# Kernel optimization log

Hardware: AMD Instinct MI355X
Metric: run time of the kernel (lower is better)

The kernel has to match this reference:

```python
import jax, jax.numpy as jnp
import numpy as np

V, E, H = 32000, 256, 256  # vocab, embed dim, encoder hidden (decoder hidden = 2H)
B, S, T = 64, 32, 32


def gru_cell(x, h, W_ih, W_hh, b_ih, b_hh):
    # PyTorch GRU cell math. x: (B, in), h: (B, Hd)
    gi = x @ W_ih.T + b_ih
    gh = h @ W_hh.T + b_hh
    i_r, i_z, i_n = jnp.split(gi, 3, axis=-1)
    h_r, h_z, h_n = jnp.split(gh, 3, axis=-1)
    r = jax.nn.sigmoid(i_r + h_r)
    z = jax.nn.sigmoid(i_z + h_z)
    n = jnp.tanh(i_n + r * h_n)
    return (1.0 - z) * n + z * h


def setup_inputs() -> dict:
    key = jax.random.key(0)
    ks = jax.random.split(key, 20)
    s = 0.05
    emb_enc = jax.random.normal(ks[0], (V, E), jnp.float32) * s
    emb_enc = emb_enc.at[0].set(0.0)  # padding_idx=0
    emb_dec = jax.random.normal(ks[1], (V, E), jnp.float32) * s
    emb_dec = emb_dec.at[0].set(0.0)
    inp = {
        "src": jax.random.randint(ks[2], (B, S), 0, V),
        "trg": jax.random.randint(ks[3], (B, T), 0, V),
        "emb_enc": emb_enc,
        # encoder bidirectional GRU (single layer)
        "W_ih_f": jax.random.normal(ks[4], (3 * H, E), jnp.float32) * s,
        "W_hh_f": jax.random.normal(ks[5], (3 * H, H), jnp.float32) * s,
        "b_ih_f": jnp.zeros((3 * H,), jnp.float32),
        "b_hh_f": jnp.zeros((3 * H,), jnp.float32),
        "W_ih_b": jax.random.normal(ks[6], (3 * H, E), jnp.float32) * s,
        "W_hh_b": jax.random.normal(ks[7], (3 * H, H), jnp.float32) * s,
        "b_ih_b": jnp.zeros((3 * H,), jnp.float32),
        "b_hh_b": jnp.zeros((3 * H,), jnp.float32),
        "emb_dec": emb_dec,
        # decoder GRU: input E + 2H, hidden 2H
        "W_ih_d": jax.random.normal(ks[8], (3 * 2 * H, E + 2 * H), jnp.float32) * s,
        "W_hh_d": jax.random.normal(ks[9], (3 * 2 * H, 2 * H), jnp.float32) * s,
        "b_ih_d": jnp.zeros((3 * 2 * H,), jnp.float32),
        "b_hh_d": jnp.zeros((3 * 2 * H,), jnp.float32),
        "fc_W": jax.random.normal(ks[10], (V, 2 * H), jnp.float32) * s,
        "fc_b": jnp.zeros((V,), jnp.float32),
    }
    return inp


def _forward(src, trg, emb_enc, W_ih_f, W_hh_f, b_ih_f, b_hh_f,
             W_ih_b, W_hh_b, b_ih_b, b_hh_b, emb_dec,
             W_ih_d, W_hh_d, b_ih_d, b_hh_d, fc_W, fc_b):
    b, s = src.shape
    t = trg.shape[1]
    x = emb_enc[src]                      # (B,S,E)
    xs = jnp.swapaxes(x, 0, 1)            # (S,B,E)
    h0 = jnp.zeros((b, H), x.dtype)

    def fstep(h, xt):
        h = gru_cell(xt, h, W_ih_f, W_hh_f, b_ih_f, b_hh_f)
        return h, None

    def bstep(h, xt):
        h = gru_cell(xt, h, W_ih_b, W_hh_b, b_ih_b, b_hh_b)
        return h, None

    hf, _ = jax.lax.scan(fstep, h0, xs)
    hb, _ = jax.lax.scan(bstep, h0, xs[::-1])
    context = jnp.concatenate([hf, hb], axis=-1)   # (B,2H) = final bidir hidden

    # teacher_forcing_ratio = 1.0 -> decoder input at step t is trg[:, t-1]
    dec_in = jnp.swapaxes(trg[:, :-1], 0, 1)       # (T-1, B)

    def dstep(h, tok):
        xt = jnp.concatenate([emb_dec[tok], context], axis=-1)  # (B, E+2H)
        h = gru_cell(xt, h, W_ih_d, W_hh_d, b_ih_d, b_hh_d)
        logits = h @ fc_W.T + fc_b                              # (B, V)
        return h, logits

    _, logits = jax.lax.scan(dstep, context, dec_in)  # (T-1, B, V)
    logits = jnp.swapaxes(logits, 0, 1)                # (B, T-1, V)
    outputs = jnp.concatenate(
        [jnp.zeros((b, 1, fc_W.shape[0]), logits.dtype), logits], axis=1)
    return outputs


def reference(src, trg, emb_enc, W_ih_f, W_hh_f, b_ih_f, b_hh_f,
              W_ih_b, W_hh_b, b_ih_b, b_hh_b, emb_dec,
              W_ih_d, W_hh_d, b_ih_d, b_hh_d, fc_W, fc_b):
    return _forward(src, trg, emb_enc, W_ih_f, W_hh_f, b_ih_f, b_hh_f,
                    W_ih_b, W_hh_b, b_ih_b, b_hh_b, emb_dec,
                    W_ih_d, W_hh_d, b_ih_d, b_hh_d, fc_W, fc_b)
```

## Files before the change

### kernel.cpp

```cpp
#include <hip/hip_runtime.h>
#include <cmath>

typedef _Float16 f16;
typedef _Float16 f16x4 __attribute__((ext_vector_type(4)));
typedef _Float16 f16x8 __attribute__((ext_vector_type(8)));
typedef float f32x4 __attribute__((ext_vector_type(4)));
typedef unsigned u32x4 __attribute__((ext_vector_type(4)));
typedef unsigned long long u64;

static constexpr u64 SENT = 0xFFFFFFFFFFFFFFFFULL;

union V4 { u32x4 u; f16x8 h; };

static constexpr size_t OFF_WIHF = 0;
static constexpr size_t OFF_WHHF = OFF_WIHF + 768UL*256*2;
static constexpr size_t OFF_WIHB = OFF_WHHF + 768UL*256*2;
static constexpr size_t OFF_WHHB = OFF_WIHB + 768UL*256*2;
static constexpr size_t OFF_WIHD = OFF_WHHB + 768UL*256*2;
static constexpr size_t OFF_WHHD = OFF_WIHD + 1536UL*768*2;
static constexpr size_t OFF_FCW  = OFF_WHHD + 1536UL*512*2;
static constexpr size_t OFF_XENC = OFF_FCW  + 32000UL*512*2;
static constexpr size_t OFF_XDEC = OFF_XENC + 2048UL*256*2;
static constexpr size_t OFF_GIF  = OFF_XDEC + 1984UL*256*2;
static constexpr size_t OFF_GIB  = OFF_GIF  + 2048UL*768*4;
static constexpr size_t OFF_GITOK= OFF_GIB  + 2048UL*768*4;
static constexpr size_t OFF_CTX32= OFF_GITOK+ 1984UL*1536*4;
static constexpr size_t OFF_CTX16= OFF_CTX32+ 64UL*512*4;
static constexpr size_t OFF_HPP  = OFF_CTX16+ 64UL*512*2;
static constexpr size_t OFF_HALL = OFF_HPP  + 2UL*32*64*256*2;

__device__ __forceinline__ float sigmoidf_(float x) {
  return __builtin_amdgcn_rcpf(1.f + __expf(-x));
}
__device__ __forceinline__ float tanhf_(float x) {
  float xc = fminf(fmaxf(x, -10.f), 10.f);
  float e = __expf(2.f * xc);
  return (e - 1.f) * __builtin_amdgcn_rcpf(e + 1.f);
}

__device__ __forceinline__ void wait_vm0() {
  asm volatile("s_waitcnt vmcnt(0)" ::: "memory");
  __builtin_amdgcn_sched_barrier(0);
}
__device__ __forceinline__ void sth4(f16* p, float a, float b, float c, float d) {
  union { u64 u; f16 h[4]; } t;
  t.h[0] = (f16)a; t.h[1] = (f16)b; t.h[2] = (f16)c; t.h[3] = (f16)d;
  __hip_atomic_store((u64*)p, t.u, __ATOMIC_RELAXED, __HIP_MEMORY_SCOPE_AGENT);
}

__global__ void k_init(const int* __restrict__ srct, const int* __restrict__ trgt,
                       const float* __restrict__ embe, const float* __restrict__ embd,
                       const float* __restrict__ wihf, const float* __restrict__ whhf,
                       const float* __restrict__ wihb, const float* __restrict__ whhb,
                       const float* __restrict__ wihd, const float* __restrict__ whhd,
                       const float* __restrict__ fcw,
                       f16* dWihf, f16* dWhhf, f16* dWihb, f16* dWhhb,
                       f16* dWihd, f16* dWhhd, f16* dFcw,
                       f16* __restrict__ Xenc, f16* __restrict__ Xdec,
                       f16* __restrict__ hpp, f16* __restrict__ Hall,
                       float* __restrict__ out) {
  int b = blockIdx.x, tid = threadIdx.x;
  if (b < 1024) {
    long t = (long)b * 256 + tid;
    const long stride = 1024L * 256;
    for (long i = t; i < 4032L * 64; i += stride) {
      int row = (int)(i >> 6), j4 = (int)(i & 63);
      const float* e; f16* d; int tok;
      if (row < 2048) {
        int s = row >> 6, bb = row & 63;
        tok = srct[bb * 32 + s]; e = embe; d = Xenc + (long)row * 256;
      } else {
        int rd = row - 2048; int tt = rd >> 6, bb = rd & 63;
        tok = trgt[bb * 32 + tt]; e = embd; d = Xdec + (long)rd * 256;
      }
      float4 v = ((const float4*)(e + (long)tok * 256))[j4];
      f16x4 o; o.x = (f16)v.x; o.y = (f16)v.y; o.z = (f16)v.z; o.w = (f16)v.w;
      ((f16x4*)d)[j4] = o;
    }
    for (long i = t; i < 64L * 8000; i += stride) {
      long bb = i / 8000, j = i % 8000;
      ((float4*)(out + bb * 1024000L))[j] = make_float4(0.f, 0.f, 0.f, 0.f);
    }
    u64* H8 = (u64*)Hall;
    if (t < 253952) H8[t] = SENT;
    u64* P8 = (u64*)hpp;
    if (t < 4096) { P8[t] = 0ULL; P8[131072 + t] = 0ULL; }
    if (t < 126976) { P8[4096 + t] = SENT; P8[131072 + 4096 + t] = SENT; }
  } else {
    long cb = b - 1024;
    const long stride = 4672L * 256;
    for (long i = cb * 256 + tid; i < 4784128L; i += stride) {
      const float* s; f16* d; long j = i;
      if (j < 49152L)        { s = wihf; d = dWihf; }
      else if (j < 98304L)   { s = whhf; d = dWhhf; j -= 49152L; }
      else if (j < 147456L)  { s = wihb; d = dWihb; j -= 98304L; }
      else if (j < 196608L)  { s = whhb; d = dWhhb; j -= 147456L; }
      else if (j < 491520L)  { s = wihd; d = dWihd; j -= 196608L; }
      else if (j < 688128L)  { s = whhd; d = dWhhd; j -= 491520L; }
      else                   { s = fcw;  d = dFcw;  j -= 688128L; }
      float4 v = ((const float4*)s)[j];
      f16x4 o; o.x = (f16)v.x; o.y = (f16)v.y; o.z = (f16)v.z; o.w = (f16)v.w;
      ((f16x4*)d)[j] = o;
    }
  }
}

__device__ __forceinline__ void gemm_body(int bx, int by,
                                          const f16* __restrict__ A, int lda,
                                          const f16* __restrict__ B, int ldb,
                                          const float* __restrict__ bias,
                                          float* __restrict__ C, int ldc, int Ksteps) {
  int m0 = bx * 64, n0 = by * 64;
  int lane = threadIdx.x & 63, w = threadIdx.x >> 6;
  int ar = m0 + w * 16 + (lane & 15);
  int koff = (lane >> 4) * 8;
  f32x4 acc[4] = {};
  for (int ks = 0; ks < Ksteps; ks++) {
    f16x8 a = *(const f16x8*)(A + (size_t)ar * lda + ks * 32 + koff);
#pragma unroll
    for (int ni = 0; ni < 4; ni++) {
      const f16* bp = B + (size_t)(n0 + ni * 16 + (lane & 15)) * ldb + ks * 32 + koff;
      f16x8 bfr = *(const f16x8*)bp;
      acc[ni] = __builtin_amdgcn_mfma_f32_16x16x32_f16(a, bfr, acc[ni], 0, 0, 0);
    }
  }
  int dm = m0 + w * 16 + ((lane >> 4) << 2);
  int dn0 = n0 + (lane & 15);
#pragma unroll
  for (int ni = 0; ni < 4; ni++) {
    int n = dn0 + ni * 16;
    float bv = bias ? bias[n] : 0.f;
#pragma unroll
    for (int r = 0; r < 4; r++) C[(size_t)(dm + r) * ldc + n] = acc[ni][r] + bv;
  }
}

__global__ __launch_bounds__(256) void k_gi(const f16* __restrict__ Xenc, const f16* __restrict__ Xdec,
                                            const f16* __restrict__ Wf, const f16* __restrict__ Wb,
                                            const f16* __restrict__ Wd,
                                            const float* __restrict__ bf, const float* __restrict__ bb,
                                            float* __restrict__ giF, float* __restrict__ giB,
                                            float* __restrict__ giTok) {
  int b = blockIdx.x;
  if (b < 384)      gemm_body(b & 31, b >> 5, Xenc, 256, Wf, 256, bf, giF, 768, 8);
  else if (b < 768) { b -= 384; gemm_body(b & 31, b >> 5, Xenc, 256, Wb, 256, bb, giB, 768, 8); }
  else              { b -= 768; gemm_body(b % 31, b / 31, Xdec, 256, Wd, 768, nullptr, giTok, 1536, 8); }
}

__global__ __launch_bounds__(256, 1) void k_enc(
    const float* __restrict__ giF, const float* __restrict__ giB,
    const f16* __restrict__ WhhF, const f16* __restrict__ WhhB,
    const float* __restrict__ bhhF, const float* __restrict__ bhhB,
    f16* __restrict__ hpp, float* __restrict__ ctx32, f16* __restrict__ ctx16) {
  __shared__ f16 W[96 * 256];
  int wg = blockIdx.x;
  int dir = wg >> 3, ns = wg & 7;
  int tid = threadIdx.x, lane = tid & 63, wv = tid >> 6;
  int mTile = wv;
  const float* gi = dir ? giB : giF;
  const f16* Whh = dir ? WhhB : WhhF;
  const float* bhh = dir ? bhhB : bhhF;
  f16* hb = hpp + (size_t)dir * (32 * 64 * 256);
  int lo = lane & 15, hi = lane >> 4;
  int m = mTile * 16 + lo;
  int jb0 = ns * 32 + hi * 4;

#pragma unroll
  for (int c = 0; c < 12; c++) {
    int seg = c * 256 + tid;
    int row = seg >> 5, ck = seg & 31;
    int q = row >> 5, ii = row & 31;
    f16x8 v = *(const f16x8*)(Whh + (size_t)(q * 256 + ns * 32 + ii) * 256 + ck * 8);
    int col = (ck * 8) ^ ((row & 7) << 3);
    *(f16x8*)&W[row * 256 + col] = v;
  }
  __syncthreads();

  float4 bh[3][2];
#pragma unroll
  for (int q = 0; q < 3; q++)
#pragma unroll
    for (int i = 0; i < 2; i++)
      bh[q][i] = *(const float4*)(bhh + q * 256 + jb0 + i * 16);

  float4 ho[2] = {};
  float4 gcur[3][2];
  {
    int s0 = dir ? 31 : 0;
    const float* g0 = gi + (size_t)s0 * (64 * 768);
#pragma unroll
    for (int q = 0; q < 3; q++)
#pragma unroll
      for (int i = 0; i < 2; i++)
        gcur[q][i] = *(const float4*)(g0 + (size_t)m * 768 + q * 256 + jb0 + i * 16);
  }

  for (int s = 0; s < 32; s++) {
    V4 hv[8];
    const char* hb8 = (const char*)hb + ((size_t)s * 16384 + (size_t)m * 256 + hi * 8) * 2;
    for (;;) {
#pragma unroll
      for (int ks = 0; ks < 8; ks++)
        asm volatile("global_load_dwordx4 %0, %1, off offset:%2 sc0 sc1"
                     : "=&v"(hv[ks].u) : "v"(hb8), "i"(ks * 64));
      wait_vm0();
      unsigned bad = 0;
#pragma unroll
      for (int ks = 0; ks < 8; ks++) {
        bad |= ((hv[ks].u.x & hv[ks].u.y) == 0xFFFFFFFFu);
        bad |= ((hv[ks].u.z & hv[ks].u.w) == 0xFFFFFFFFu);
      }
      if (!__any((int)bad)) break;
      __builtin_amdgcn_s_sleep(1);
    }
    f32x4 acc[3][2] = {};
#pragma unroll
    for (int ks = 0; ks < 8; ks++) {
#pragma unroll
      for (int q = 0; q < 3; q++)
#pragma unroll
        for (int i = 0; i < 2; i++) {
          int row = q * 32 + i * 16 + lo;
          int col = (ks * 32 + hi * 8) ^ ((row & 7) << 3);
          f16x8 w = *(const f16x8*)&W[row * 256 + col];
          acc[q][i] = __builtin_amdgcn_mfma_f32_16x16x32_f16(w, hv[ks].h, acc[q][i], 0, 0, 0);
        }
    }
#pragma unroll
    for (int i = 0; i < 2; i++) {
      float hvv[4];
#pragma unroll
      for (int r2 = 0; r2 < 4; r2++) {
        float rg = sigmoidf_(((const float*)&gcur[0][i])[r2] + acc[0][i][r2] + ((const float*)&bh[0][i])[r2]);
        float zg = sigmoidf_(((const float*)&gcur[1][i])[r2] + acc[1][i][r2] + ((const float*)&bh[1][i])[r2]);
        float ng = tanhf_(((const float*)&gcur[2][i])[r2] + rg * (acc[2][i][r2] + ((const float*)&bh[2][i])[r2]));
        float hprev = ((const float*)&ho[i])[r2];
        hvv[r2] = (1.f - zg) * ng + zg * hprev;
        ((float*)&ho[i])[r2] = hvv[r2];
      }
      if (s < 31) sth4(hb + (size_t)(s + 1) * 16384 + m * 256 + jb0 + i * 16,
                       hvv[0], hvv[1], hvv[2], hvv[3]);
    }
    if (s < 31) {
      int sn = s + 1;
      int sgin = dir ? (31 - sn) : sn;
      const float* gs = gi + (size_t)sgin * (64 * 768);
#pragma unroll
      for (int q = 0; q < 3; q++)
#pragma unroll
        for (int i = 0; i < 2; i++)
          gcur[q][i] = *(const float4*)(gs + (size_t)m * 768 + q * 256 + jb0 + i * 16);
    }
  }
#pragma unroll
  for (int i = 0; i < 2; i++) {
    int c = dir * 256 + jb0 + i * 16;
    *(float4*)(ctx32 + m * 512 + c) = ho[i];
    union { u64 u; f16 h[4]; } t;
#pragma unroll
    for (int r2 = 0; r2 < 4; r2++) t.h[r2] = (f16)((const float*)&ho[i])[r2];
    *(u64*)(ctx16 + m * 512 + c) = t.u;
  }
}

__global__ __launch_bounds__(256, 1) void k_dec(
    const float* __restrict__ giTok, const f16* __restrict__ Wihd, const float* __restrict__ bihd,
    const f16* __restrict__ Whh, const float* __restrict__ bhh,
    const float* __restrict__ ctx32, const f16* __restrict__ ctx16,
    f16* __restrict__ Hall) {
  __shared__ f16 W[48 * 512];
  int cg = blockIdx.x;
  int tid = threadIdx.x, lane = tid & 63, wv = tid >> 6;
  int mTile = wv;
  int lo = lane & 15, hi = lane >> 4;
  int koff = hi * 8;
  int m = mTile * 16 + lo;
  int j0 = cg * 16 + hi * 4;

#pragma unroll
  for (int c = 0; c < 12; c++) {
    int seg = c * 256 + tid;
    int row = seg >> 6, ck = seg & 63;
    int q = row >> 4, ii = row & 15;
    f16x8 v = *(const f16x8*)(Whh + (size_t)(q * 512 + cg * 16 + ii) * 512 + ck * 8);
    int col = (ck * 8) ^ ((row & 7) << 3);
    *(f16x8*)&W[row * 512 + col] = v;
  }

  f32x4 acx[3] = {};
#pragma unroll
  for (int ks = 0; ks < 16; ks++) {
    f16x8 a = *(const f16x8*)(ctx16 + (size_t)m * 512 + ks * 32 + koff);
#pragma unroll
    for (int q = 0; q < 3; q++) {
      f16x8 w = *(const f16x8*)(Wihd + (size_t)(q * 512 + cg * 16 + lo) * 768 + 256 + ks * 32 + koff);
      acx[q] = __builtin_amdgcn_mfma_f32_16x16x32_f16(w, a, acx[q], 0, 0, 0);
    }
  }
  float b0[4], b1[4], bo2[4], bhn[4];
#pragma unroll
  for (int r2 = 0; r2 < 4; r2++) {
    b0[r2]  = acx[0][r2] + bihd[j0 + r2]        + bhh[j0 + r2];
    b1[r2]  = acx[1][r2] + bihd[512 + j0 + r2]  + bhh[512 + j0 + r2];
    bo2[r2] = acx[2][r2] + bihd[1024 + j0 + r2];
    bhn[r2] = bhh[1024 + j0 + r2];
  }
  float4 ho = *(const float4*)(ctx32 + m * 512 + j0);
  float4 gcur[3];
#pragma unroll
  for (int q = 0; q < 3; q++)
    gcur[q] = *(const float4*)(giTok + (size_t)m * 1536 + q * 512 + j0);
  __syncthreads();

  for (int t = 0; t < 31; t++) {
    V4 hv[16];
    if (t == 0) {
      const char* cb = (const char*)ctx16 + ((size_t)m * 512 + hi * 8) * 2;
#pragma unroll
      for (int ks = 0; ks < 16; ks++)
        hv[ks].u = *(const u32x4*)(cb + ks * 64);
    } else {
      const char* hb8 = (const char*)Hall + ((size_t)(t - 1) * 32768 + (size_t)m * 512 + hi * 8) * 2;
      for (;;) {
#pragma unroll
        for (int ks = 0; ks < 16; ks++)
          asm volatile("global_load_dwordx4 %0, %1, off offset:%2 sc0 sc1"
                       : "=&v"(hv[ks].u) : "v"(hb8), "i"(ks * 64));
        wait_vm0();
        unsigned bad = 0;
#pragma unroll
        for (int ks = 0; ks < 16; ks++) {
          bad |= ((hv[ks].u.x & hv[ks].u.y) == 0xFFFFFFFFu);
          bad |= ((hv[ks].u.z & hv[ks].u.w) == 0xFFFFFFFFu);
        }
        if (!__any((int)bad)) break;
        __builtin_amdgcn_s_sleep(1);
      }
    }
    f32x4 acc[3] = {};
#pragma unroll
    for (int ks = 0; ks < 16; ks++) {
#pragma unroll
      for (int q = 0; q < 3; q++) {
        int row = q * 16 + lo;
        int col = (ks * 32 + hi * 8) ^ ((row & 7) << 3);
        f16x8 w = *(const f16x8*)&W[row * 512 + col];
        acc[q] = __builtin_amdgcn_mfma_f32_16x16x32_f16(w, hv[ks].h, acc[q], 0, 0, 0);
      }
    }
    float hvv[4];
#pragma unroll
    for (int r2 = 0; r2 < 4; r2++) {
      float rg = sigmoidf_(((const float*)&gcur[0])[r2] + acc[0][r2] + b0[r2]);
      float zg = sigmoidf_(((const float*)&gcur[1])[r2] + acc[1][r2] + b1[r2]);
      float ng = tanhf_(((const float*)&gcur[2])[r2] + bo2[r2] + rg * (acc[2][r2] + bhn[r2]));
      float hprev = ((const float*)&ho)[r2];
      hvv[r2] = (1.f - zg) * ng + zg * hprev;
      ((float*)&ho)[r2] = hvv[r2];
    }
    sth4(Hall + (size_t)t * 32768 + (size_t)m * 512 + j0, hvv[0], hvv[1], hvv[2], hvv[3]);
    {
      int tn = (t + 1 < 31) ? t + 1 : 30;
      const float* gs = giTok + (size_t)tn * (64 * 1536);
#pragma unroll
      for (int q = 0; q < 3; q++)
        gcur[q] = *(const float4*)(gs + (size_t)m * 1536 + q * 512 + j0);
    }
  }
}

__global__ __launch_bounds__(256, 2) void k_fc(const f16* __restrict__ Hall, const f16* __restrict__ Wfc,
                                               const float* __restrict__ fcb, float* __restrict__ out) {
  __shared__ f16 As[128 * 64];
  __shared__ f16 Bs[128 * 64];
  int bid = blockIdx.x;
  int bx = bid >> 4;
  int by = bid & 15;
  int m0 = by * 128, n0 = bx * 128;
  int tid = threadIdx.x, lane = tid & 63, wv = tid >> 6;
  int wm = wv >> 1, wn = wv & 1;
  f32x4 acc[4][4] = {};
  for (int kk = 0; kk < 8; kk++) {
    f16x8 ra[4], rb[4];
#pragma unroll
    for (int c = 0; c < 4; c++) {
      int seg = c * 256 + tid;
      int row = seg >> 3, ko = (seg & 7) * 8;
      ra[c] = *(const f16x8*)(Hall + (size_t)(m0 + row) * 512 + kk * 64 + ko);
      rb[c] = *(const f16x8*)(Wfc + (size_t)(n0 + row) * 512 + kk * 64 + ko);
    }
    __syncthreads();
#pragma unroll
    for (int c = 0; c < 4; c++) {
      int seg = c * 256 + tid;
      int row = seg >> 3;
      int col = ((seg & 7) * 8) ^ ((row & 7) << 3);
      *(f16x8*)&As[row * 64 + col] = ra[c];
      *(f16x8*)&Bs[row * 64 + col] = rb[c];
    }
    __syncthreads();
#pragma unroll
    for (int ks = 0; ks < 2; ks++) {
      f16x8 af[4], bf[4];
#pragma unroll
      for (int mi = 0; mi < 4; mi++) {
        int row = wm * 64 + mi * 16 + (lane & 15);
        int col = (ks * 32 + (lane >> 4) * 8) ^ ((row & 7) << 3);
        af[mi] = *(const f16x8*)&As[row * 64 + col];
      }
#pragma unroll
      for (int ni = 0; ni < 4; ni++) {
        int row = wn * 64 + ni * 16 + (lane & 15);
        int col = (ks * 32 + (lane >> 4) * 8) ^ ((row & 7) << 3);
        bf[ni] = *(const f16x8*)&Bs[row * 64 + col];
      }
#pragma unroll
      for (int mi = 0; mi < 4; mi++) {
#pragma unroll
        for (int ni = 0; ni < 4; ni++)
          acc[mi][ni] = __builtin_amdgcn_mfma_f32_16x16x32_f16(af[mi], bf[ni], acc[mi][ni], 0, 0, 0);
      }
    }
  }
  int dn0 = n0 + wn * 64 + (lane & 15);
  float bv[4];
#pragma unroll
  for (int ni = 0; ni < 4; ni++) bv[ni] = fcb[dn0 + ni * 16];
#pragma unroll
  for (int mi = 0; mi < 4; mi++) {
    int mbase = m0 + wm * 64 + mi * 16 + ((lane >> 4) << 2);
#pragma unroll
    for (int rr = 0; rr < 4; rr++) {
      int mm = mbase + rr;
      if (mm < 1984) {
        int t = mm >> 6, bb = mm & 63;
        float* orow = out + (size_t)bb * 1024000 + (size_t)(t + 1) * 32000;
#pragma unroll
        for (int ni = 0; ni < 4; ni++)
          __builtin_nontemporal_store(acc[mi][ni][rr] + bv[ni], orow + dn0 + ni * 16);
      }
    }
  }
}

extern "C" void kernel_launch(void* const* d_in, const int* in_sizes, int n_in,
                              void* d_out, int out_size, void* d_ws, size_t ws_size,
                              hipStream_t stream) {
  const int*   srct = (const int*)d_in[0];
  const int*   trgt = (const int*)d_in[1];
  const float* embe = (const float*)d_in[2];
  const float* wihf = (const float*)d_in[3];
  const float* whhf = (const float*)d_in[4];
  const float* bihf = (const float*)d_in[5];
  const float* bhhf = (const float*)d_in[6];
  const float* wihb = (const float*)d_in[7];
  const float* whhb = (const float*)d_in[8];
  const float* bihb = (const float*)d_in[9];
  const float* bhhb = (const float*)d_in[10];
  const float* embd = (const float*)d_in[11];
  const float* wihd = (const float*)d_in[12];
  const float* whhd = (const float*)d_in[13];
  const float* bihd = (const float*)d_in[14];
  const float* bhhd = (const float*)d_in[15];
  const float* fcw  = (const float*)d_in[16];
  const float* fcb  = (const float*)d_in[17];
  float* out = (float*)d_out;
  char* ws = (char*)d_ws;

  f16* W_ihf = (f16*)(ws + OFF_WIHF);
  f16* W_hhf = (f16*)(ws + OFF_WHHF);
  f16* W_ihb = (f16*)(ws + OFF_WIHB);
  f16* W_hhb = (f16*)(ws + OFF_WHHB);
  f16* W_ihd = (f16*)(ws + OFF_WIHD);
  f16* W_hhd = (f16*)(ws + OFF_WHHD);
  f16* Wfc   = (f16*)(ws + OFF_FCW);
  f16* Xenc  = (f16*)(ws + OFF_XENC);
  f16* Xdec  = (f16*)(ws + OFF_XDEC);
  float* giF   = (float*)(ws + OFF_GIF);
  float* giB   = (float*)(ws + OFF_GIB);
  float* giTok = (float*)(ws + OFF_GITOK);
  float* ctx32 = (float*)(ws + OFF_CTX32);
  f16*   ctx16 = (f16*)(ws + OFF_CTX16);
  f16*   hpp   = (f16*)(ws + OFF_HPP);
  f16*   Hall  = (f16*)(ws + OFF_HALL);

  k_init<<<5696, 256, 0, stream>>>(srct, trgt, embe, embd,
                                   wihf, whhf, wihb, whhb, wihd, whhd, fcw,
                                   W_ihf, W_hhf, W_ihb, W_hhb, W_ihd, W_hhd, Wfc,
                                   Xenc, Xdec, hpp, Hall, out);
  k_gi<<<1512, 256, 0, stream>>>(Xenc, Xdec, W_ihf, W_ihb, W_ihd, bihf, bihb,
                                 giF, giB, giTok);
  k_enc<<<16, 256, 0, stream>>>(giF, giB, W_hhf, W_hhb, bhhf, bhhb, hpp, ctx32, ctx16);
  k_dec<<<32, 256, 0, stream>>>(giTok, W_ihd, bihd, W_hhd, bhhd, ctx32, ctx16, Hall);
  k_fc<<<4000, 256, 0, stream>>>(Hall, Wfc, fcb, out);
}
```

Baseline: 425.8 us.

## Add lightweight spin probes to recurrences and use direct global-to-LDS loads in FC GEMM

```diff
diff --git a/kernel.cpp b/kernel.cpp
--- a/kernel.cpp
+++ b/kernel.cpp
@@ -11,6 +11,9 @@
 static constexpr u64 SENT = 0xFFFFFFFFFFFFFFFFULL;
 
 union V4 { u32x4 u; f16x8 h; };
+
+typedef __attribute__((address_space(3))) void lds_t;
+typedef const __attribute__((address_space(1))) void gbl_t;
 
 static constexpr size_t OFF_WIHF = 0;
 static constexpr size_t OFF_WHHF = OFF_WIHF + 768UL*256*2;
@@ -195,7 +198,21 @@
         gcur[q][i] = *(const float4*)(g0 + (size_t)m * 768 + q * 256 + jb0 + i * 16);
   }
 
+  const int pj = lane >> 3;
+  const int prow = mTile * 16 + (lane & 7);
+
   for (int s = 0; s < 32; s++) {
+    {
+      const u64* gp = (const u64*)(hb + (size_t)s * 16384) + (size_t)prow * 64 + pj * 8;
+      for (;;) {
+        u64 v;
+        asm volatile("global_load_dwordx2 %0, %1, off sc0 sc1" : "=v"(v) : "v"(gp));
+        asm volatile("s_waitcnt vmcnt(0)" ::: "memory");
+        if (__all((int)(v != SENT))) break;
+        __builtin_amdgcn_s_sleep(1);
+      }
+      __builtin_amdgcn_sched_barrier(0);
+    }
     V4 hv[8];
     const char* hb8 = (const char*)hb + ((size_t)s * 16384 + (size_t)m * 256 + hi * 8) * 2;
     for (;;) {
@@ -312,6 +329,9 @@
     gcur[q] = *(const float4*)(giTok + (size_t)m * 1536 + q * 512 + j0);
   __syncthreads();
 
+  const int pj = lane >> 1;
+  const int prow = mTile * 16 + (lane & 1) * 8;
+
   for (int t = 0; t < 31; t++) {
     V4 hv[16];
     if (t == 0) {
@@ -320,6 +340,17 @@
       for (int ks = 0; ks < 16; ks++)
         hv[ks].u = *(const u32x4*)(cb + ks * 64);
     } else {
+      {
+        const u64* gp = (const u64*)(Hall + (size_t)(t - 1) * 32768) + (size_t)prow * 128 + pj * 4;
+        for (;;) {
+          u64 v;
+          asm volatile("global_load_dwordx2 %0, %1, off sc0 sc1" : "=v"(v) : "v"(gp));
+          asm volatile("s_waitcnt vmcnt(0)" ::: "memory");
+          if (__all((int)(v != SENT))) break;
+          __builtin_amdgcn_s_sleep(1);
+        }
+        __builtin_amdgcn_sched_barrier(0);
+      }
       const char* hb8 = (const char*)Hall + ((size_t)(t - 1) * 32768 + (size_t)m * 512 + hi * 8) * 2;
       for (;;) {
 #pragma unroll
@@ -379,41 +410,29 @@
   int m0 = by * 128, n0 = bx * 128;
   int tid = threadIdx.x, lane = tid & 63, wv = tid >> 6;
   int wm = wv >> 1, wn = wv & 1;
+  int lo = lane & 15, hi = lane >> 4;
+  int srow = lane >> 3, scol = (lane & 7) * 8;
   f32x4 acc[4][4] = {};
   for (int kk = 0; kk < 8; kk++) {
-    f16x8 ra[4], rb[4];
-#pragma unroll
-    for (int c = 0; c < 4; c++) {
-      int seg = c * 256 + tid;
-      int row = seg >> 3, ko = (seg & 7) * 8;
-      ra[c] = *(const f16x8*)(Hall + (size_t)(m0 + row) * 512 + kk * 64 + ko);
-      rb[c] = *(const f16x8*)(Wfc + (size_t)(n0 + row) * 512 + kk * 64 + ko);
-    }
-    __syncthreads();
-#pragma unroll
-    for (int c = 0; c < 4; c++) {
-      int seg = c * 256 + tid;
-      int row = seg >> 3;
-      int col = ((seg & 7) * 8) ^ ((row & 7) << 3);
-      *(f16x8*)&As[row * 64 + col] = ra[c];
-      *(f16x8*)&Bs[row * 64 + col] = rb[c];
+    if (kk) __syncthreads();
+#pragma unroll
+    for (int c4 = 0; c4 < 4; c4++) {
+      int c = wv * 4 + c4;
+      const f16* sA = Hall + (size_t)(m0 + c * 8 + srow) * 512 + kk * 64 + scol;
+      const f16* sB = Wfc  + (size_t)(n0 + c * 8 + srow) * 512 + kk * 64 + scol;
+      __builtin_amdgcn_global_load_lds((gbl_t*)sA, (lds_t*)&As[c * 512], 16, 0, 0);
+      __builtin_amdgcn_global_load_lds((gbl_t*)sB, (lds_t*)&Bs[c * 512], 16, 0, 0);
     }
     __syncthreads();
 #pragma unroll
     for (int ks = 0; ks < 2; ks++) {
       f16x8 af[4], bf[4];
 #pragma unroll
-      for (int mi = 0; mi < 4; mi++) {
-        int row = wm * 64 + mi * 16 + (lane & 15);
-        int col = (ks * 32 + (lane >> 4) * 8) ^ ((row & 7) << 3);
-        af[mi] = *(const f16x8*)&As[row * 64 + col];
-      }
-#pragma unroll
-      for (int ni = 0; ni < 4; ni++) {
-        int row = wn * 64 + ni * 16 + (lane & 15);
-        int col = (ks * 32 + (lane >> 4) * 8) ^ ((row & 7) << 3);
-        bf[ni] = *(const f16x8*)&Bs[row * 64 + col];
-      }
+      for (int mi = 0; mi < 4; mi++)
+        af[mi] = *(const f16x8*)&As[(wm * 64 + mi * 16 + lo) * 64 + ks * 32 + hi * 8];
+#pragma unroll
+      for (int ni = 0; ni < 4; ni++)
+        bf[ni] = *(const f16x8*)&Bs[(wn * 64 + ni * 16 + lo) * 64 + ks * 32 + hi * 8];
 #pragma unroll
       for (int mi = 0; mi < 4; mi++) {
 #pragma unroll
@@ -422,13 +441,13 @@
       }
     }
   }
-  int dn0 = n0 + wn * 64 + (lane & 15);
+  int dn0 = n0 + wn * 64 + lo;
   float bv[4];
 #pragma unroll
   for (int ni = 0; ni < 4; ni++) bv[ni] = fcb[dn0 + ni * 16];
 #pragma unroll
   for (int mi = 0; mi < 4; mi++) {
-    int mbase = m0 + wm * 64 + mi * 16 + ((lane >> 4) << 2);
+    int mbase = m0 + wm * 64 + mi * 16 + (hi << 2);
 #pragma unroll
     for (int rr = 0; rr < 4; rr++) {
       int mm = mbase + rr;
```

New measurement: 445.5 us. 4.6% more time.
